# Kernel optimization log

Measured on AMD Instinct MI355X. Metric: run time of the kernel, lower is better.

The kernel has to match this reference:

```python
import jax, jax.numpy as jnp
import numpy as np

T, B, IN, HID, NL = 256, 256, 64, 512, 2
LS = HID // NL  # per-layer hidden size of GRUCellStack


def setup_inputs() -> dict:
    key = jax.random.key(0)
    ks = jax.random.split(key, 9)
    w = lambda k, shape: (jax.random.normal(k, shape, jnp.float32) * 0.05)
    return {
        "obs": jax.random.normal(ks[0], (T, B, IN), jnp.float32),
        "reset": jax.random.randint(ks[1], (T, B), 0, 2).astype(bool),
        "h": jnp.zeros((B, HID), jnp.float32),
        "W_lin": w(ks[2], (HID, IN)),
        "b_lin": jnp.zeros((HID,), jnp.float32),
        "w_ih0": w(ks[3], (3 * LS, HID)),
        "w_hh0": w(ks[4], (3 * LS, LS)),
        "b_ih0": jnp.zeros((3 * LS,), jnp.float32),
        "b_hh0": jnp.zeros((3 * LS,), jnp.float32),
        "w_ih1": w(ks[5], (3 * LS, LS)),
        "w_hh1": w(ks[6], (3 * LS, LS)),
        "b_ih1": jnp.zeros((3 * LS,), jnp.float32),
        "b_hh1": jnp.zeros((3 * LS,), jnp.float32),
    }


def _gru_cell(i_gates, h, w_hh, b_hh):
    # PyTorch nn.GRUCell math; i_gates = x @ w_ih.T + b_ih precomputed.
    h_gates = h @ w_hh.T + b_hh
    ir, iz, in_ = jnp.split(i_gates, 3, axis=-1)
    hr, hz, hn = jnp.split(h_gates, 3, axis=-1)
    r = jax.nn.sigmoid(ir + hr)
    z = jax.nn.sigmoid(iz + hz)
    n = jnp.tanh(in_ + r * hn)
    return (1.0 - z) * n + z * h


def reference(obs, reset, h, W_lin, b_lin, w_ih0, w_hh0, b_ih0, b_hh0,
              w_ih1, w_hh1, b_ih1, b_hh1):
    # embed all timesteps at once: [T,B,HID]
    x = obs.astype(jnp.float32) @ W_lin.T + b_lin
    # layer-0 input-side gates depend only on x -> precompute: [T,B,3*LS]
    ig0 = x @ w_ih0.T + b_ih0
    mask = (~reset).astype(jnp.float32)[..., None]  # [T,B,1]

    def step(hc, inp):
        ig0_t, m_t = inp
        hc = hc * m_t                      # reset masking of full stacked state
        h0, h1 = jnp.split(hc, 2, axis=-1)  # per-layer states [B,LS]
        h0n = _gru_cell(ig0_t, h0, w_hh0, b_hh0)
        ig1 = h0n @ w_ih1.T + b_ih1
        h1n = _gru_cell(ig1, h1, w_hh1, b_hh1)
        hn = jnp.concatenate([h0n, h1n], axis=-1)  # [B,HID]
        return hn, hn

    _, states_h = jax.lax.scan(step, h, (ig0, mask))
    return states_h  # [T,B,HID]
```

## Files before the change

kernel.cpp:

```cpp
#include <hip/hip_runtime.h>

#define T_    256
#define B_    256
#define IN_   64
#define HID_  512
#define LS_   256
#define G3_   768
#define TBS_  32
#define MBT_  64
#define WP_   264
#define FSTRIDE_ 128

typedef short bf16x8v __attribute__((ext_vector_type(8)));
typedef float f32x4  __attribute__((ext_vector_type(4)));
typedef unsigned long long u64;

#define MFMA_B16(A, B, C) __builtin_amdgcn_mfma_f32_16x16x32_bf16(A, B, C, 0, 0, 0)

__device__ __forceinline__ unsigned short f2bf(float f) {
  union { float f; unsigned u; } v; v.f = f;
  unsigned r = v.u + 0x7fffu + ((v.u >> 16) & 1u);
  return (unsigned short)(r >> 16);
}
__device__ __forceinline__ float sigm(float x) { return 1.0f / (1.0f + __expf(-x)); }
__device__ __forceinline__ float tanh_f(float x) {
  x = fminf(fmaxf(x, -15.0f), 15.0f);
  float e = __expf(-2.0f * x);
  return (1.0f - e) / (1.0f + e);
}

__device__ __forceinline__ void st2_coh(unsigned short* p, unsigned short v) {
  __hip_atomic_store(p, v, __ATOMIC_RELAXED, __HIP_MEMORY_SCOPE_AGENT);
}
__device__ __forceinline__ bf16x8v ld16_coh(const unsigned short* p) {
  union { u64 q[2]; bf16x8v v; } u;
  u.q[0] = __hip_atomic_load((const u64*)p,     __ATOMIC_RELAXED, __HIP_MEMORY_SCOPE_AGENT);
  u.q[1] = __hip_atomic_load((const u64*)(p+4), __ATOMIC_RELAXED, __HIP_MEMORY_SCOPE_AGENT);
  return u.v;
}

__global__ void prep_conv(const float* __restrict__ whh0, const float* __restrict__ wih1,
                          const float* __restrict__ whh1, const unsigned char* __restrict__ rst,
                          unsigned short* __restrict__ dst, int* __restrict__ flagp,
                          int* __restrict__ flags) {
  const int idx = blockIdx.x * blockDim.x + threadIdx.x;
  const int N1 = G3_ * LS_;
  if (idx < 3 * N1) {
    float v;
    if (idx < N1)            v = whh0[idx];
    else if (idx < 2 * N1)   v = wih1[idx - N1];
    else                     v = whh1[idx - 2 * N1];
    dst[idx] = f2bf(v);
  }
  if (blockIdx.x == 1 && threadIdx.x < 64) {
    int tm = threadIdx.x & 31;
    flags[tm * FSTRIDE_ + ((threadIdx.x & 32) ? 64 : 0)] = 0;
  }
  if (blockIdx.x == 0) {
    __shared__ int f;
    if (threadIdx.x == 0) f = 0;
    __syncthreads();
    int any = 0;
    for (int i = 0; i < 8; ++i) {
      int off = threadIdx.x * 8 + i;
      if ((off & 3) && rst[off]) any = 1;
    }
    if (any) atomicOr(&f, 1);
    __syncthreads();
    if (threadIdx.x == 0) *flagp = f;
  }
}

__global__ void prep_wc(const float* __restrict__ W_lin, const float* __restrict__ b_lin,
                        const float* __restrict__ w_ih0, const float* __restrict__ b_ih0,
                        unsigned short* __restrict__ wc, float* __restrict__ bc) {
  const int n = blockIdx.x;
  const int i = threadIdx.x;
  const float* wrow = w_ih0 + (size_t)n * HID_;
  float acc = 0.f;
  for (int h = 0; h < HID_; ++h) acc += wrow[h] * W_lin[h * IN_ + i];
  wc[n * IN_ + i] = f2bf(acc);
  float pb = 0.f;
  for (int h = i; h < HID_; h += 64) pb += wrow[h] * b_lin[h];
  __shared__ float red[64];
  red[i] = pb;
  __syncthreads();
  if (i == 0) {
    float s = 0.f;
    for (int k = 0; k < 64; ++k) s += red[k];
    bc[n] = s + b_ih0[n];
  }
}

__global__ __launch_bounds__(512, 2) void gru_main(
    const float* __restrict__ obs, const unsigned char* __restrict__ rst,
    const float* __restrict__ h_init,
    const unsigned short* __restrict__ wc,
    const unsigned short* __restrict__ whh0g,
    const unsigned short* __restrict__ wih1g, const unsigned short* __restrict__ whh1g,
    const float* __restrict__ bcp, const float* __restrict__ bhh0,
    const float* __restrict__ bih1, const float* __restrict__ bhh1,
    const int* __restrict__ flagp, int* __restrict__ flag0, int* __restrict__ flag1,
    unsigned short* __restrict__ hx0, unsigned short* __restrict__ hx1,
    float* __restrict__ out) {

  __shared__ __align__(16) unsigned short wlds[3 * 96 * WP_];
  __shared__ int s_sm[64];
  __shared__ int s_start_sh;

  const int tid  = threadIdx.x;
  const int lane = tid & 63;
  const int wave = tid >> 6;
  const int l15  = lane & 15;
  const int quad = lane >> 4;
  const int mt   = wave & 3;
  const int c16  = (wave >> 2) * 16;

  const int x  = blockIdx.x;
  const int cx = x & 7, m8 = x >> 3;
  const int j  = m8 & 7;
  const int team = cx * 4 + (m8 >> 3);
  const int bg = team & 3, tc = team >> 2;
  const int b0 = bg * MBT_, t0 = tc * TBS_;

  int* f0 = flag0 + team * FSTRIDE_;
  int* f1 = flag1 + team * FSTRIDE_;

  const int flag = *flagp;
#define RVAL(i) (rst[flag ? (i) : ((i) << 2)] != 0)

#pragma unroll
  for (int q = 0; q < 3; ++q) {
    const unsigned short* src = (q == 0) ? whh0g : (q == 1) ? wih1g : whh1g;
    for (int cid = tid; cid < 96 * 32; cid += 512) {
      int lr = cid >> 5, off8 = (cid & 31) * 8;
      int g = lr >> 5, cc = lr & 31;
      int grow = (g << 8) + (j << 5) + cc;
      *(f32x4*)&wlds[(q * 96 + lr) * WP_ + off8] =
          *(const f32x4*)&src[(size_t)grow * 256 + off8];
    }
  }

  const int colg = j * 32 + c16 + l15;
  const float b0r = bcp[colg] + bhh0[colg];
  const float b0z = bcp[256 + colg] + bhh0[256 + colg];
  const float b0i = bcp[512 + colg];
  const float b0h = bhh0[512 + colg];
  const float b1r = bih1[colg] + bhh1[colg];
  const float b1z = bih1[256 + colg] + bhh1[256 + colg];
  const float b1i = bih1[512 + colg];
  const float b1h = bhh1[512 + colg];

  if (tid < 64) {
    int s = 0;
    for (int tt = t0; tt >= 1; --tt) {
      if (RVAL(tt * B_ + b0 + tid)) { s = tt; break; }
    }
    s_sm[tid] = s;
  }
  __syncthreads();
  if (tid == 0) {
    int s = s_sm[0];
    for (int k = 1; k < 64; ++k) s = s < s_sm[k] ? s : s_sm[k];
    s_start_sh = s;
  }
  __syncthreads();
  const int s_start = s_start_sh;

  bf16x8v h0A[8], h1A[8];
  const bf16x8v z8 = {0, 0, 0, 0, 0, 0, 0, 0};
#pragma unroll
  for (int kc = 0; kc < 8; ++kc) { h0A[kc] = z8; h1A[kc] = z8; }
  float h0v[4] = {0.f, 0.f, 0.f, 0.f}, h1v[4] = {0.f, 0.f, 0.f, 0.f};
  if (s_start == 0) {
    const float* hrow = h_init + (size_t)(b0 + mt * 16 + l15) * HID_;
#pragma unroll
    for (int kc = 0; kc < 8; ++kc) {
      f32x4 u0 = *(const f32x4*)(hrow + kc * 32 + quad * 8);
      f32x4 u1 = *(const f32x4*)(hrow + kc * 32 + quad * 8 + 4);
      f32x4 v0 = *(const f32x4*)(hrow + 256 + kc * 32 + quad * 8);
      f32x4 v1 = *(const f32x4*)(hrow + 256 + kc * 32 + quad * 8 + 4);
      bf16x8v a, b;
#pragma unroll
      for (int e = 0; e < 4; ++e) {
        a[e] = (short)f2bf(u0[e]); a[4 + e] = (short)f2bf(u1[e]);
        b[e] = (short)f2bf(v0[e]); b[4 + e] = (short)f2bf(v1[e]);
      }
      h0A[kc] = a; h1A[kc] = b;
    }
#pragma unroll
    for (int r = 0; r < 4; ++r) {
      const int m = mt * 16 + quad * 4 + r;
      h0v[r] = h_init[(size_t)(b0 + m) * HID_ + colg];
      h1v[r] = h_init[(size_t)(b0 + m) * HID_ + 256 + colg];
    }
  }

  const unsigned short* wR0 = &wlds[(0 * 96 + 0 * 32 + c16 + l15) * WP_];
  const unsigned short* wZ0 = &wlds[(0 * 96 + 1 * 32 + c16 + l15) * WP_];
  const unsigned short* wN0 = &wlds[(0 * 96 + 2 * 32 + c16 + l15) * WP_];
  const unsigned short* iR1 = &wlds[(1 * 96 + 0 * 32 + c16 + l15) * WP_];
  const unsigned short* iZ1 = &wlds[(1 * 96 + 1 * 32 + c16 + l15) * WP_];
  const unsigned short* iN1 = &wlds[(1 * 96 + 2 * 32 + c16 + l15) * WP_];
  const unsigned short* hR1 = &wlds[(2 * 96 + 0 * 32 + c16 + l15) * WP_];
  const unsigned short* hZ1 = &wlds[(2 * 96 + 1 * 32 + c16 + l15) * WP_];
  const unsigned short* hN1 = &wlds[(2 * 96 + 2 * 32 + c16 + l15) * WP_];

  f32x4 ou0a, ou0b, ou1a, ou1b;
  {
    const float* po = obs + ((size_t)s_start * B_ + b0 + mt * 16 + l15) * IN_;
    ou0a = __builtin_nontemporal_load((const f32x4*)(po + quad * 8));
    ou0b = __builtin_nontemporal_load((const f32x4*)(po + quad * 8 + 4));
    ou1a = __builtin_nontemporal_load((const f32x4*)(po + 32 + quad * 8));
    ou1b = __builtin_nontemporal_load((const f32x4*)(po + 32 + quad * 8 + 4));
  }

  for (int t = s_start; t < t0 + TBS_; ++t) {
    const int  kk = t - s_start + 1;
    const bool wr = (t >= t0);
    const bool rs0 = RVAL(t * B_ + b0 + mt * 16 + l15);
    bool rse[4];
#pragma unroll
    for (int r = 0; r < 4; ++r) rse[r] = RVAL(t * B_ + b0 + mt * 16 + quad * 4 + r);

    f32x4 ar = {0.f, 0.f, 0.f, 0.f}, az = ar, ani = ar, anh = ar;
    {
#pragma unroll
      for (int kc = 0; kc < 2; ++kc) {
        f32x4 u0 = kc ? ou1a : ou0a;
        f32x4 u1 = kc ? ou1b : ou0b;
        bf16x8v oA;
#pragma unroll
        for (int e = 0; e < 4; ++e) { oA[e] = (short)f2bf(u0[e]); oA[4 + e] = (short)f2bf(u1[e]); }
        const size_t wo = (size_t)colg * 64 + kc * 32 + quad * 8;
        bf16x8v br = *(const bf16x8v*)&wc[wo];
        bf16x8v bz = *(const bf16x8v*)&wc[wo + (size_t)256 * 64];
        bf16x8v bn = *(const bf16x8v*)&wc[wo + (size_t)512 * 64];
        ar  = MFMA_B16(oA, br, ar);
        az  = MFMA_B16(oA, bz, az);
        ani = MFMA_B16(oA, bn, ani);
      }
    }
#pragma unroll
    for (int kc = 0; kc < 8; ++kc) {
      bf16x8v am = rs0 ? z8 : h0A[kc];
      const int o = kc * 32 + quad * 8;
      ar  = MFMA_B16(am, *(const bf16x8v*)&wR0[o], ar);
      az  = MFMA_B16(am, *(const bf16x8v*)&wZ0[o], az);
      anh = MFMA_B16(am, *(const bf16x8v*)&wN0[o], anh);
    }
    {
      unsigned short* hw = hx0 + ((size_t)team * 2 + (kk & 1)) * (MBT_ * 256);
#pragma unroll
      for (int r = 0; r < 4; ++r) {
        const int m = mt * 16 + quad * 4 + r;
        float rr = sigm(ar[r] + b0r);
        float zz = sigm(az[r] + b0z);
        float nn = tanh_f(ani[r] + b0i + rr * (anh[r] + b0h));
        float hp = rse[r] ? 0.f : h0v[r];
        float hv = (1.f - zz) * nn + zz * hp;
        h0v[r] = hv;
        st2_coh(hw + m * 256 + colg, f2bf(hv));
        if (wr) __builtin_nontemporal_store(hv, &out[((size_t)t * B_ + b0 + m) * HID_ + colg]);
      }
    }
    __syncthreads();
    if (tid == 0) {
      __hip_atomic_fetch_add(f0, 1, __ATOMIC_RELAXED, __HIP_MEMORY_SCOPE_AGENT);
      int cap = 0;
      while (__hip_atomic_load(f0, __ATOMIC_RELAXED, __HIP_MEMORY_SCOPE_AGENT)
                 < 8 * kk && cap < (1 << 16)) { __builtin_amdgcn_s_sleep(2); ++cap; }
      if (kk >= 2) {
        cap = 0;
        while (__hip_atomic_load(f1, __ATOMIC_RELAXED, __HIP_MEMORY_SCOPE_AGENT)
                   < 8 * (kk - 1) && cap < (1 << 16)) { __builtin_amdgcn_s_sleep(2); ++cap; }
      }
    }
    __syncthreads();
    {
      const int tn = (t + 1 < t0 + TBS_) ? t + 1 : t;
      const float* po = obs + ((size_t)tn * B_ + b0 + mt * 16 + l15) * IN_;
      ou0a = __builtin_nontemporal_load((const f32x4*)(po + quad * 8));
      ou0b = __builtin_nontemporal_load((const f32x4*)(po + quad * 8 + 4));
      ou1a = __builtin_nontemporal_load((const f32x4*)(po + 32 + quad * 8));
      ou1b = __builtin_nontemporal_load((const f32x4*)(po + 32 + quad * 8 + 4));
    }
    {
      const unsigned short* hr0 =
          hx0 + ((size_t)team * 2 + (kk & 1)) * (MBT_ * 256) + (mt * 16 + l15) * 256;
#pragma unroll
      for (int kc = 0; kc < 8; ++kc)
        h0A[kc] = ld16_coh(hr0 + kc * 32 + quad * 8);
      if (kk >= 2) {
        const unsigned short* hr1 =
            hx1 + ((size_t)team * 2 + ((kk - 1) & 1)) * (MBT_ * 256) + (mt * 16 + l15) * 256;
#pragma unroll
        for (int kc = 0; kc < 8; ++kc)
          h1A[kc] = ld16_coh(hr1 + kc * 32 + quad * 8);
      }
    }

    ar = (f32x4){0.f, 0.f, 0.f, 0.f}; az = ar; ani = ar; anh = ar;
#pragma unroll
    for (int kc = 0; kc < 8; ++kc) {
      bf16x8v ai_ = h0A[kc];
      bf16x8v am  = rs0 ? z8 : h1A[kc];
      const int o = kc * 32 + quad * 8;
      ar  = MFMA_B16(ai_, *(const bf16x8v*)&iR1[o], ar);
      az  = MFMA_B16(ai_, *(const bf16x8v*)&iZ1[o], az);
      ani = MFMA_B16(ai_, *(const bf16x8v*)&iN1[o], ani);
      ar  = MFMA_B16(am, *(const bf16x8v*)&hR1[o], ar);
      az  = MFMA_B16(am, *(const bf16x8v*)&hZ1[o], az);
      anh = MFMA_B16(am, *(const bf16x8v*)&hN1[o], anh);
    }
    {
      unsigned short* hw = hx1 + ((size_t)team * 2 + (kk & 1)) * (MBT_ * 256);
#pragma unroll
      for (int r = 0; r < 4; ++r) {
        const int m = mt * 16 + quad * 4 + r;
        float rr = sigm(ar[r] + b1r);
        float zz = sigm(az[r] + b1z);
        float nn = tanh_f(ani[r] + b1i + rr * (anh[r] + b1h));
        float hp = rse[r] ? 0.f : h1v[r];
        float hv = (1.f - zz) * nn + zz * hp;
        h1v[r] = hv;
        st2_coh(hw + m * 256 + colg, f2bf(hv));
        if (wr) __builtin_nontemporal_store(hv, &out[((size_t)t * B_ + b0 + m) * HID_ + 256 + colg]);
      }
    }
    __syncthreads();
    if (tid == 0)
      __hip_atomic_fetch_add(f1, 1, __ATOMIC_RELAXED, __HIP_MEMORY_SCOPE_AGENT);
  }
#undef RVAL
}

extern "C" void kernel_launch(void* const* d_in, const int* in_sizes, int n_in,
                              void* d_out, int out_size, void* d_ws, size_t ws_size,
                              hipStream_t stream) {
  const float* obs    = (const float*)d_in[0];
  const unsigned char* rst = (const unsigned char*)d_in[1];
  const float* h_init = (const float*)d_in[2];
  const float* W_lin  = (const float*)d_in[3];
  const float* b_lin  = (const float*)d_in[4];
  const float* w_ih0  = (const float*)d_in[5];
  const float* w_hh0  = (const float*)d_in[6];
  const float* b_ih0  = (const float*)d_in[7];
  const float* b_hh0  = (const float*)d_in[8];
  const float* w_ih1  = (const float*)d_in[9];
  const float* w_hh1  = (const float*)d_in[10];
  const float* b_ih1  = (const float*)d_in[11];
  const float* b_hh1  = (const float*)d_in[12];

  char* w = (char*)d_ws;
  unsigned short* wcp   = (unsigned short*)(w);
  unsigned short* whh0b = (unsigned short*)(w + 98304);
  unsigned short* wih1b = (unsigned short*)(w + 491520);
  unsigned short* whh1b = (unsigned short*)(w + 884736);
  float*          bcp   = (float*)(w + 1277952);
  int*            flagp = (int*)(w + 1281024);
  int*            flags = (int*)(w + 1281088);
  unsigned short* hx0   = (unsigned short*)(w + 1310720);
  unsigned short* hx1   = (unsigned short*)(w + 1310720 + 2097152);

  prep_conv<<<1152, 512, 0, stream>>>(w_hh0, w_ih1, w_hh1, rst, whh0b, flagp, flags);
  prep_wc<<<768, 64, 0, stream>>>(W_lin, b_lin, w_ih0, b_ih0, wcp, bcp);
  gru_main<<<256, 512, 0, stream>>>(obs, rst, h_init, wcp, whh0b, wih1b, whh1b,
                                    bcp, b_hh0, b_ih1, b_hh1, flagp,
                                    flags, flags + 64, hx0, hx1, (float*)d_out);
}
```

Baseline: 714.0 us.

## Merge per-step layer barriers into one flag and defer output stores past it

Drops the separate layer-1 completion flag and its spin-wait. The kernel now relies on the single layer-0 flag: it is incremented after the previous step's layer-1 state was written, so waiting on it also covers that state. Global output stores for layer 0 and the lagged layer-1 step move after the barrier and the hidden-state loads, so they overlap with the wait and the next compute; the final layer-1 step is stored after the loop. This removes one cross-block sync round per timestep. In exchange, correctness depends on program-order visibility under relaxed atomics.

```diff
diff --git a/kernel.cpp b/kernel.cpp
--- a/kernel.cpp
+++ b/kernel.cpp
@@ -52,9 +52,8 @@
     else                     v = whh1[idx - 2 * N1];
     dst[idx] = f2bf(v);
   }
-  if (blockIdx.x == 1 && threadIdx.x < 64) {
-    int tm = threadIdx.x & 31;
-    flags[tm * FSTRIDE_ + ((threadIdx.x & 32) ? 64 : 0)] = 0;
+  if (blockIdx.x == 1 && threadIdx.x < 32) {
+    flags[threadIdx.x * FSTRIDE_] = 0;
   }
   if (blockIdx.x == 0) {
     __shared__ int f;
@@ -100,7 +99,7 @@
     const unsigned short* __restrict__ wih1g, const unsigned short* __restrict__ whh1g,
     const float* __restrict__ bcp, const float* __restrict__ bhh0,
     const float* __restrict__ bih1, const float* __restrict__ bhh1,
-    const int* __restrict__ flagp, int* __restrict__ flag0, int* __restrict__ flag1,
+    const int* __restrict__ flagp, int* __restrict__ flag0,
     unsigned short* __restrict__ hx0, unsigned short* __restrict__ hx1,
     float* __restrict__ out) {
 
@@ -124,7 +123,6 @@
   const int b0 = bg * MBT_, t0 = tc * TBS_;
 
   int* f0 = flag0 + team * FSTRIDE_;
-  int* f1 = flag1 + team * FSTRIDE_;
 
   const int flag = *flagp;
 #define RVAL(i) (rst[flag ? (i) : ((i) << 2)] != 0)
@@ -261,7 +259,6 @@
         float hv = (1.f - zz) * nn + zz * hp;
         h0v[r] = hv;
         st2_coh(hw + m * 256 + colg, f2bf(hv));
-        if (wr) __builtin_nontemporal_store(hv, &out[((size_t)t * B_ + b0 + m) * HID_ + colg]);
       }
     }
     __syncthreads();
@@ -270,13 +267,37 @@
       int cap = 0;
       while (__hip_atomic_load(f0, __ATOMIC_RELAXED, __HIP_MEMORY_SCOPE_AGENT)
                  < 8 * kk && cap < (1 << 16)) { __builtin_amdgcn_s_sleep(2); ++cap; }
+    }
+    __syncthreads();
+    {
+      const unsigned short* hr0 =
+          hx0 + ((size_t)team * 2 + (kk & 1)) * (MBT_ * 256) + (mt * 16 + l15) * 256;
+#pragma unroll
+      for (int kc = 0; kc < 8; ++kc)
+        h0A[kc] = ld16_coh(hr0 + kc * 32 + quad * 8);
       if (kk >= 2) {
-        cap = 0;
-        while (__hip_atomic_load(f1, __ATOMIC_RELAXED, __HIP_MEMORY_SCOPE_AGENT)
-                   < 8 * (kk - 1) && cap < (1 << 16)) { __builtin_amdgcn_s_sleep(2); ++cap; }
-      }
-    }
-    __syncthreads();
+        const unsigned short* hr1 =
+            hx1 + ((size_t)team * 2 + ((kk - 1) & 1)) * (MBT_ * 256) + (mt * 16 + l15) * 256;
+#pragma unroll
+        for (int kc = 0; kc < 8; ++kc)
+          h1A[kc] = ld16_coh(hr1 + kc * 32 + quad * 8);
+      }
+    }
+    if (wr) {
+#pragma unroll
+      for (int r = 0; r < 4; ++r) {
+        const int m = mt * 16 + quad * 4 + r;
+        __builtin_nontemporal_store(h0v[r], &out[((size_t)t * B_ + b0 + m) * HID_ + colg]);
+      }
+    }
+    if (t - 1 >= t0) {
+#pragma unroll
+      for (int r = 0; r < 4; ++r) {
+        const int m = mt * 16 + quad * 4 + r;
+        __builtin_nontemporal_store(h1v[r],
+            &out[((size_t)(t - 1) * B_ + b0 + m) * HID_ + 256 + colg]);
+      }
+    }
     {
       const int tn = (t + 1 < t0 + TBS_) ? t + 1 : t;
       const float* po = obs + ((size_t)tn * B_ + b0 + mt * 16 + l15) * IN_;
@@ -284,20 +305,6 @@
       ou0b = __builtin_nontemporal_load((const f32x4*)(po + quad * 8 + 4));
       ou1a = __builtin_nontemporal_load((const f32x4*)(po + 32 + quad * 8));
       ou1b = __builtin_nontemporal_load((const f32x4*)(po + 32 + quad * 8 + 4));
-    }
-    {
-      const unsigned short* hr0 =
-          hx0 + ((size_t)team * 2 + (kk & 1)) * (MBT_ * 256) + (mt * 16 + l15) * 256;
-#pragma unroll
-      for (int kc = 0; kc < 8; ++kc)
-        h0A[kc] = ld16_coh(hr0 + kc * 32 + quad * 8);
-      if (kk >= 2) {
-        const unsigned short* hr1 =
-            hx1 + ((size_t)team * 2 + ((kk - 1) & 1)) * (MBT_ * 256) + (mt * 16 + l15) * 256;
-#pragma unroll
-        for (int kc = 0; kc < 8; ++kc)
-          h1A[kc] = ld16_coh(hr1 + kc * 32 + quad * 8);
-      }
     }
 
     ar = (f32x4){0.f, 0.f, 0.f, 0.f}; az = ar; ani = ar; anh = ar;
@@ -325,12 +332,17 @@
         float hv = (1.f - zz) * nn + zz * hp;
         h1v[r] = hv;
         st2_coh(hw + m * 256 + colg, f2bf(hv));
-        if (wr) __builtin_nontemporal_store(hv, &out[((size_t)t * B_ + b0 + m) * HID_ + 256 + colg]);
-      }
-    }
-    __syncthreads();
-    if (tid == 0)
-      __hip_atomic_fetch_add(f1, 1, __ATOMIC_RELAXED, __HIP_MEMORY_SCOPE_AGENT);
+      }
+    }
+  }
+  {
+    const int tl = t0 + TBS_ - 1;
+#pragma unroll
+    for (int r = 0; r < 4; ++r) {
+      const int m = mt * 16 + quad * 4 + r;
+      __builtin_nontemporal_store(h1v[r],
+          &out[((size_t)tl * B_ + b0 + m) * HID_ + 256 + colg]);
+    }
   }
 #undef RVAL
 }
@@ -367,5 +379,5 @@
   prep_wc<<<768, 64, 0, stream>>>(W_lin, b_lin, w_ih0, b_ih0, wcp, bcp);
   gru_main<<<256, 512, 0, stream>>>(obs, rst, h_init, wcp, whh0b, wih1b, whh1b,
                                     bcp, b_hh0, b_ih1, b_hh1, flagp,
-                                    flags, flags + 64, hx0, hx1, (float*)d_out);
-}
+                                    flags, hx0, hx1, (float*)d_out);
+}
```

Result: faster. 658.2 us (-7.8%).
